# Kernel tuning notes

Hardware: AMD Instinct MI355X
Metric: run time of the kernel (lower is better)

Reference implementation:

```python
import jax, jax.numpy as jnp
import numpy as np

B, N, C, H = 16, 4096, 256, 4
D = C // H

def setup_inputs() -> dict:
    key = jax.random.key(0)
    ks = jax.random.split(key, 8)
    w = 0.01  # small init, mimics xavier_uniform gain=0.1
    x = jax.random.normal(ks[0], (B, N, C), jnp.float32)
    S = jax.random.normal(ks[1], (B, H, D, D), jnp.float32) * 0.1
    Wq = jax.random.normal(ks[2], (C, C), jnp.float32) * w
    Wk = jax.random.normal(ks[3], (C, C), jnp.float32) * w
    Wv = jax.random.normal(ks[4], (C, C), jnp.float32) * w
    Wb = jax.random.normal(ks[5], (H, C), jnp.float32) * w  # beta_proj (zeros in torch init; random for nontrivial math)
    Wo = jax.random.normal(ks[6], (C, C), jnp.float32) * w
    g_rms = jnp.ones((C,), jnp.float32)
    return {"x": x, "S": S, "Wq": Wq, "Wk": Wk, "Wv": Wv, "Wb": Wb, "Wo": Wo, "g_rms": g_rms}

def reference(x, S, Wq, Wk, Wv, Wb, Wo, g_rms):
    b, n, c = x.shape
    h = Wb.shape[0]
    d = c // h
    # projections -> (B,H,N,D)
    q = (x @ Wq.T).reshape(b, n, h, d).transpose(0, 2, 1, 3)
    k = (x @ Wk.T).reshape(b, n, h, d).transpose(0, 2, 1, 3)
    v = (x @ Wv.T).reshape(b, n, h, d).transpose(0, 2, 1, 3)
    # feature map + L2 normalize keys
    k = jax.nn.elu(k) + 1.0
    k = k / (jnp.linalg.norm(k, axis=-1, keepdims=True) + 1e-6)
    # per-head gates (B,H,N,1)
    beta = jax.nn.sigmoid(jnp.einsum('bnc,hc->bhn', x, Wb))[..., None]
    # decay + state read
    Sd = S * 0.95
    y = jnp.einsum('bhij,bhnj->bhni', Sd, q)
    pred = jnp.einsum('bhij,bhnj->bhni', Sd, k)
    # delta-rule write: outer(mean weighted error, mean key)
    w_err = jnp.mean(beta * (v - pred), axis=2)  # (B,H,D)
    w_key = jnp.mean(k, axis=2)                  # (B,H,D)
    S_new = jnp.clip(Sd + jnp.einsum('bhi,bhj->bhij', w_err, w_key), -10.0, 10.0)
    # merge heads, RMSNorm, output projection
    y = y.transpose(0, 2, 1, 3).reshape(b, n, c)
    y = y * jax.lax.rsqrt(jnp.mean(y * y, axis=-1, keepdims=True) + 1e-6) * g_rms
    out = y @ Wo.T
    return out, S_new
```

## Files before the change

kernel.cpp:

```cpp
#include <hip/hip_runtime.h>
#include <math.h>


typedef _Float16 f16;
typedef f16 f16x8 __attribute__((ext_vector_type(8)));
typedef f16 f16x4 __attribute__((ext_vector_type(4)));
typedef float f32x4 __attribute__((ext_vector_type(4)));

typedef const __attribute__((address_space(1))) void gvoid;
typedef __attribute__((address_space(3))) void svoid;

__device__ __forceinline__ void gload16(const void* g, void* l) {
  __builtin_amdgcn_global_load_lds((gvoid*)g, (svoid*)l, 16, 0, 0);
}

__device__ __forceinline__ f16x8 cvt8(const float* q) {
  float4 a = *(const float4*)q;
  float4 b = *(const float4*)(q + 4);
  f16x8 r;
  r[0] = (f16)a.x; r[1] = (f16)a.y; r[2] = (f16)a.z; r[3] = (f16)a.w;
  r[4] = (f16)b.x; r[5] = (f16)b.y; r[6] = (f16)b.z; r[7] = (f16)b.w;
  return r;
}

__global__ __launch_bounds__(256) void prep_w(
    const float* __restrict__ Wk, const float* __restrict__ Wo,
    const float* __restrict__ g, f16* __restrict__ Wkh,
    f16* __restrict__ Wogh) {
  int i = blockIdx.x * 256 + threadIdx.x;
#pragma unroll
  for (int j = 0; j < 4; ++j) {
    int idx = i + j * 16384;
    Wkh[idx] = (f16)Wk[idx];
    Wogh[idx] = (f16)(Wo[idx] * g[idx & 255]);
  }
}

__global__ __launch_bounds__(256) void beta_xbsum_h(
    const float* __restrict__ x, const float* __restrict__ Wb,
    float* __restrict__ betaArr, float* __restrict__ xbsum,
    f16* __restrict__ xh) {
  const int t = threadIdx.x;
  const int wave = t >> 6, lane = t & 63;
  const int b = blockIdx.x >> 6;
  const int tile = blockIdx.x & 63;
  float4 wb[4];
#pragma unroll
  for (int h = 0; h < 4; ++h) wb[h] = *(const float4*)(Wb + h * 256 + lane * 4);
  float xacc[4][4] = {};
  const size_t rowbase = (size_t)b * 4096 + tile * 64;
  __shared__ float bsh[4][64];
  float4 xv = *(const float4*)(x + (rowbase + wave) * 256 + lane * 4);
#pragma unroll 2
  for (int i = 0; i < 16; ++i) {
    int r = i * 4 + wave;
    float4 nx = xv;
    if (i < 15)
      nx = *(const float4*)(x + (rowbase + r + 4) * 256 + lane * 4);
    f16x4 hx;
    hx[0] = (f16)xv.x; hx[1] = (f16)xv.y; hx[2] = (f16)xv.z; hx[3] = (f16)xv.w;
    *(f16x4*)(xh + (rowbase + r) * 256 + lane * 4) = hx;
#pragma unroll
    for (int h = 0; h < 4; ++h) {
      float s = xv.x * wb[h].x + xv.y * wb[h].y + xv.z * wb[h].z + xv.w * wb[h].w;
#pragma unroll
      for (int off = 32; off; off >>= 1) s += __shfl_xor(s, off);
      float bh = 1.f / (1.f + __expf(-s));
      if (lane == h) bsh[h][r] = bh;
      xacc[h][0] += bh * xv.x; xacc[h][1] += bh * xv.y;
      xacc[h][2] += bh * xv.z; xacc[h][3] += bh * xv.w;
    }
    xv = nx;
  }
  __shared__ float xbp[4][4][256];
#pragma unroll
  for (int h = 0; h < 4; ++h)
#pragma unroll
    for (int j = 0; j < 4; ++j) xbp[wave][h][lane * 4 + j] = xacc[h][j];
  __syncthreads();
  {
    int h = t >> 6, r = t & 63;
    betaArr[((size_t)(b * 4 + h) << 12) + tile * 64 + r] = bsh[h][r];
  }
  for (int idx = t; idx < 1024; idx += 256) {
    int h = idx >> 8, c = idx & 255;
    float s = xbp[0][h][c] + xbp[1][h][c] + xbp[2][h][c] + xbp[3][h][c];
    atomicAdd(&xbsum[(b * 4 + h) * 256 + c], s);
  }
}

__global__ __launch_bounds__(256) void kgemm_h(
    const f16* __restrict__ xh, const f16* __restrict__ Wkh,
    const float* __restrict__ betaArr,
    float* __restrict__ ksum, float* __restrict__ kbsum) {
  __shared__ union {
    struct { f16 A[128][64]; f16 B[128][64]; } s;
    f16 K[128][128];
  } u;
  __shared__ float bstage[2][128];
  const int t = threadIdx.x;
  const int m0 = blockIdx.y * 128;
  const int n0 = blockIdx.x * 128;
  const int b = m0 >> 12;
  const int wave = t >> 6, lane = t & 63;
  const int wm = (wave >> 1) * 64, wn = (wave & 1) * 64;
  const int fr = lane & 15, fq = lane >> 4;
  const int fr7 = fr & 7;
  const int srow = lane >> 3;
  const int sc = (lane & 7) ^ srow;
  {
    int hh = t >> 7, r = t & 127;
    bstage[hh][r] =
        betaArr[((size_t)(b * 4 + (n0 >> 6) + hh) << 12) + (m0 & 4095) + r];
  }
  const char* Ab = (const char*)&u.s.A[0][0];
  const char* Bb = (const char*)&u.s.B[0][0];
  f32x4 acc[4][4] = {};
#pragma unroll 1
  for (int kt = 0; kt < 4; ++kt) {
    const int k0 = kt * 64;
#pragma unroll
    for (int j = 0; j < 4; ++j) {
      int c = j * 4 + wave;
      int row = c * 8 + srow;
      gload16(xh + (size_t)(m0 + row) * 256 + k0 + sc * 8, &u.s.A[0][0] + c * 512);
      gload16(Wkh + (size_t)(n0 + row) * 256 + k0 + sc * 8, &u.s.B[0][0] + c * 512);
    }
    __syncthreads();
#pragma unroll
    for (int ks = 0; ks < 2; ++ks) {
      const int p = ((ks * 4 + fq) ^ fr7) << 4;
      f16x8 afr[4], bfr[4];
#pragma unroll
      for (int mi = 0; mi < 4; ++mi)
        afr[mi] = *(const f16x8*)(Ab + (wm + mi * 16 + fr) * 128 + p);
#pragma unroll
      for (int ni = 0; ni < 4; ++ni)
        bfr[ni] = *(const f16x8*)(Bb + (wn + ni * 16 + fr) * 128 + p);
#pragma unroll
      for (int mi = 0; mi < 4; ++mi)
#pragma unroll
        for (int ni = 0; ni < 4; ++ni)
          acc[mi][ni] = __builtin_amdgcn_mfma_f32_16x16x32_f16(
              afr[mi], bfr[ni], acc[mi][ni], 0, 0, 0);
    }
    __syncthreads();
  }
#pragma unroll
  for (int mi = 0; mi < 4; ++mi)
#pragma unroll
    for (int rr = 0; rr < 4; ++rr) {
      float s = 0.f;
#pragma unroll
      for (int ni = 0; ni < 4; ++ni) {
        float v = acc[mi][ni][rr];
        v = v > 0.f ? v + 1.f : __expf(v);
        acc[mi][ni][rr] = v;
        s += v * v;
      }
#pragma unroll
      for (int off = 1; off < 16; off <<= 1) s += __shfl_xor(s, off);
      float inv = 1.f / (sqrtf(s) + 1e-6f);
#pragma unroll
      for (int ni = 0; ni < 4; ++ni) acc[mi][ni][rr] *= inv;
    }
#pragma unroll
  for (int mi = 0; mi < 4; ++mi)
#pragma unroll
    for (int ni = 0; ni < 4; ++ni)
#pragma unroll
      for (int rr = 0; rr < 4; ++rr)
        u.K[wm + mi * 16 + fq * 4 + rr][wn + ni * 16 + fr] = (f16)acc[mi][ni][rr];
  __syncthreads();
  if (t < 128) {
    const int c = t, hl = c >> 6;
    float sk = 0.f, skb = 0.f;
#pragma unroll 4
    for (int r = 0; r < 128; ++r) {
      float v = (float)u.K[r][c];
      float be = bstage[hl][r];
      sk += v;
      skb += be * v;
    }
    int gh = b * 4 + (n0 >> 6) + hl;
    atomicAdd(&ksum[gh * 64 + (c & 63)], sk);
    atomicAdd(&kbsum[gh * 64 + (c & 63)], skb);
  }
}

__global__ __launch_bounds__(256) void fold_M(
    const float* __restrict__ S, const float* __restrict__ Wq,
    f16* __restrict__ M) {
  const int bh = blockIdx.y;
  const int dq = blockIdx.x;
  const int h = bh & 3;
  const int t = threadIdx.x;
  const float* Sp = S + (size_t)bh * 4096 + dq * 8 * 64;
  const float* Wp = Wq + (size_t)h * 64 * 256 + t;
  float m[8] = {};
#pragma unroll 4
  for (int e = 0; e < 64; ++e) {
    float wv = Wp[e * 256];
#pragma unroll
    for (int dd = 0; dd < 8; ++dd) m[dd] += Sp[dd * 64 + e] * wv;
  }
  f16* Mb = M + (size_t)(bh >> 2) * 65536;
#pragma unroll
  for (int dd = 0; dd < 8; ++dd)
    Mb[(size_t)(h * 64 + dq * 8 + dd) * 256 + t] = (f16)(0.95f * m[dd]);
}

__global__ __launch_bounds__(256) void ygemm_h(
    const f16* __restrict__ xh, int m_base, const f16* __restrict__ M,
    f16* __restrict__ y, float* __restrict__ rowssq) {
  __shared__ f16 As[128][64];
  __shared__ f16 Bs[128][64];
  const int t = threadIdx.x;
  const int m0 = blockIdx.y * 128;
  const int n0 = blockIdx.x * 128;
  const int b = (m_base + m0) >> 12;
  const f16* Mb = M + (size_t)b * 65536;
  const int wave = t >> 6, lane = t & 63;
  const int wm = (wave >> 1) * 64, wn = (wave & 1) * 64;
  const int fr = lane & 15, fq = lane >> 4;
  const int fr7 = fr & 7;
  const int srow = lane >> 3;
  const int sc = (lane & 7) ^ srow;
  const char* Ab = (const char*)&As[0][0];
  const char* Bb = (const char*)&Bs[0][0];
  f32x4 acc[4][4] = {};
#pragma unroll 1
  for (int kt = 0; kt < 4; ++kt) {
    const int k0 = kt * 64;
#pragma unroll
    for (int j = 0; j < 4; ++j) {
      int c = j * 4 + wave;
      int row = c * 8 + srow;
      gload16(xh + (size_t)(m_base + m0 + row) * 256 + k0 + sc * 8,
              &As[0][0] + c * 512);
      gload16(Mb + (size_t)(n0 + row) * 256 + k0 + sc * 8, &Bs[0][0] + c * 512);
    }
    __syncthreads();
#pragma unroll
    for (int ks = 0; ks < 2; ++ks) {
      const int p = ((ks * 4 + fq) ^ fr7) << 4;
      f16x8 afr[4], bfr[4];
#pragma unroll
      for (int mi = 0; mi < 4; ++mi)
        afr[mi] = *(const f16x8*)(Ab + (wm + mi * 16 + fr) * 128 + p);
#pragma unroll
      for (int ni = 0; ni < 4; ++ni)
        bfr[ni] = *(const f16x8*)(Bb + (wn + ni * 16 + fr) * 128 + p);
#pragma unroll
      for (int mi = 0; mi < 4; ++mi)
#pragma unroll
        for (int ni = 0; ni < 4; ++ni)
          acc[mi][ni] = __builtin_amdgcn_mfma_f32_16x16x32_f16(
              afr[mi], bfr[ni], acc[mi][ni], 0, 0, 0);
    }
    __syncthreads();
  }
#pragma unroll
  for (int mi = 0; mi < 4; ++mi)
#pragma unroll
    for (int rr = 0; rr < 4; ++rr) {
      float s = 0.f;
#pragma unroll
      for (int ni = 0; ni < 4; ++ni) {
        float v = acc[mi][ni][rr];
        s += v * v;
        int row = m0 + wm + mi * 16 + fq * 4 + rr;
        int col = n0 + wn + ni * 16 + fr;
        y[(size_t)row * 256 + col] = (f16)v;
      }
#pragma unroll
      for (int off = 1; off < 16; off <<= 1) s += __shfl_xor(s, off);
      if (fr == 0)
        atomicAdd(&rowssq[m0 + wm + mi * 16 + fq * 4 + rr], s);
    }
}

__global__ __launch_bounds__(256) void ogemm_h(
    const f16* __restrict__ y, const float* __restrict__ rowssq,
    const f16* __restrict__ Wogh, float* __restrict__ out, int m_base) {
  __shared__ f16 As[128][64];
  __shared__ f16 Bs[128][64];
  __shared__ float rsl[128];
  const int t = threadIdx.x;
  const int m0 = blockIdx.y * 128;
  const int n0 = blockIdx.x * 128;
  const int wave = t >> 6, lane = t & 63;
  const int wm = (wave >> 1) * 64, wn = (wave & 1) * 64;
  const int fr = lane & 15, fq = lane >> 4;
  const int fr7 = fr & 7;
  const int srow = lane >> 3;
  const int sc = (lane & 7) ^ srow;
  const char* Ab = (const char*)&As[0][0];
  const char* Bb = (const char*)&Bs[0][0];
  if (t < 128) rsl[t] = rsqrtf(rowssq[m0 + t] * (1.f / 256.f) + 1e-6f);
  f32x4 acc[4][4] = {};
#pragma unroll 1
  for (int kt = 0; kt < 4; ++kt) {
    const int k0 = kt * 64;
#pragma unroll
    for (int j = 0; j < 4; ++j) {
      int c = j * 4 + wave;
      int row = c * 8 + srow;
      gload16(y + (size_t)(m0 + row) * 256 + k0 + sc * 8, &As[0][0] + c * 512);
      gload16(Wogh + (size_t)(n0 + row) * 256 + k0 + sc * 8, &Bs[0][0] + c * 512);
    }
    __syncthreads();
#pragma unroll
    for (int ks = 0; ks < 2; ++ks) {
      const int p = ((ks * 4 + fq) ^ fr7) << 4;
      f16x8 afr[4], bfr[4];
#pragma unroll
      for (int mi = 0; mi < 4; ++mi)
        afr[mi] = *(const f16x8*)(Ab + (wm + mi * 16 + fr) * 128 + p);
#pragma unroll
      for (int ni = 0; ni < 4; ++ni)
        bfr[ni] = *(const f16x8*)(Bb + (wn + ni * 16 + fr) * 128 + p);
#pragma unroll
      for (int mi = 0; mi < 4; ++mi)
#pragma unroll
        for (int ni = 0; ni < 4; ++ni)
          acc[mi][ni] = __builtin_amdgcn_mfma_f32_16x16x32_f16(
              afr[mi], bfr[ni], acc[mi][ni], 0, 0, 0);
    }
    __syncthreads();
  }
#pragma unroll
  for (int mi = 0; mi < 4; ++mi)
#pragma unroll
    for (int rr = 0; rr < 4; ++rr) {
      int lrow = wm + mi * 16 + fq * 4 + rr;
      float rs = rsl[lrow];
#pragma unroll
      for (int ni = 0; ni < 4; ++ni) {
        int row = m_base + m0 + lrow;
        int col = n0 + wn + ni * 16 + fr;
        out[(size_t)row * 256 + col] = rs * acc[mi][ni][rr];
      }
    }
}

__global__ __launch_bounds__(256) void beta_xbsum(
    const float* __restrict__ x, const float* __restrict__ Wb,
    float* __restrict__ betaArr, float* __restrict__ xbsum) {
  const int t = threadIdx.x;
  const int wave = t >> 6, lane = t & 63;
  const int b = blockIdx.x >> 6;
  const int tile = blockIdx.x & 63;
  float4 wb[4];
#pragma unroll
  for (int h = 0; h < 4; ++h) wb[h] = *(const float4*)(Wb + h * 256 + lane * 4);
  float xacc[4][4] = {};
  const size_t rowbase = (size_t)b * 4096 + tile * 64;
  __shared__ float bsh[4][64];
  float4 xv = *(const float4*)(x + (rowbase + wave) * 256 + lane * 4);
#pragma unroll 2
  for (int i = 0; i < 16; ++i) {
    int r = i * 4 + wave;
    float4 nx = xv;
    if (i < 15)
      nx = *(const float4*)(x + (rowbase + r + 4) * 256 + lane * 4);
#pragma unroll
    for (int h = 0; h < 4; ++h) {
      float s = xv.x * wb[h].x + xv.y * wb[h].y + xv.z * wb[h].z + xv.w * wb[h].w;
#pragma unroll
      for (int off = 32; off; off >>= 1) s += __shfl_xor(s, off);
      float bh = 1.f / (1.f + __expf(-s));
      if (lane == h) bsh[h][r] = bh;
      xacc[h][0] += bh * xv.x; xacc[h][1] += bh * xv.y;
      xacc[h][2] += bh * xv.z; xacc[h][3] += bh * xv.w;
    }
    xv = nx;
  }
  __shared__ float xbp[4][4][256];
#pragma unroll
  for (int h = 0; h < 4; ++h)
#pragma unroll
    for (int j = 0; j < 4; ++j) xbp[wave][h][lane * 4 + j] = xacc[h][j];
  __syncthreads();
  {
    int h = t >> 6, r = t & 63;
    betaArr[((size_t)(b * 4 + h) << 12) + tile * 64 + r] = bsh[h][r];
  }
  for (int idx = t; idx < 1024; idx += 256) {
    int h = idx >> 8, c = idx & 255;
    float s = xbp[0][h][c] + xbp[1][h][c] + xbp[2][h][c] + xbp[3][h][c];
    atomicAdd(&xbsum[(b * 4 + h) * 256 + c], s);
  }
}

__global__ __launch_bounds__(256) void kgemm_sums(
    const float* __restrict__ x, const float* __restrict__ Wk,
    const float* __restrict__ betaArr,
    float* __restrict__ ksum, float* __restrict__ kbsum) {
  __shared__ union {
    struct { f16 A[128][72]; f16 B[128][72]; } s;
    f16 K[128][132];
  } u;
  __shared__ float bstage[2][128];
  const int t = threadIdx.x;
  const int m0 = blockIdx.y * 128;
  const int n0 = blockIdx.x * 128;
  const int b = m0 >> 12;
  const int wave = t >> 6, lane = t & 63;
  const int wm = (wave >> 1) * 64, wn = (wave & 1) * 64;
  const int fr = lane & 15, fq = lane >> 4;
  {
    int hh = t >> 7, r = t & 127;
    bstage[hh][r] =
        betaArr[((size_t)(b * 4 + (n0 >> 6) + hh) << 12) + (m0 & 4095) + r];
  }
  f32x4 acc[4][4] = {};
#pragma unroll 1
  for (int kt = 0; kt < 4; ++kt) {
    const int k0 = kt * 64;
#pragma unroll
    for (int i = 0; i < 4; ++i) {
      int id = i * 256 + t;
      int row = id >> 3, cc = id & 7;
      *(f16x8*)&u.s.A[row][cc * 8] =
          cvt8(x + (size_t)(m0 + row) * 256 + k0 + cc * 8);
      *(f16x8*)&u.s.B[row][cc * 8] =
          cvt8(Wk + (size_t)(n0 + row) * 256 + k0 + cc * 8);
    }
    __syncthreads();
#pragma unroll
    for (int ks = 0; ks < 2; ++ks) {
      f16x8 afr[4], bfr[4];
#pragma unroll
      for (int mi = 0; mi < 4; ++mi)
        afr[mi] = *(const f16x8*)&u.s.A[wm + mi * 16 + fr][ks * 32 + fq * 8];
#pragma unroll
      for (int ni = 0; ni < 4; ++ni)
        bfr[ni] = *(const f16x8*)&u.s.B[wn + ni * 16 + fr][ks * 32 + fq * 8];
#pragma unroll
      for (int mi = 0; mi < 4; ++mi)
#pragma unroll
        for (int ni = 0; ni < 4; ++ni)
          acc[mi][ni] = __builtin_amdgcn_mfma_f32_16x16x32_f16(
              afr[mi], bfr[ni], acc[mi][ni], 0, 0, 0);
    }
    __syncthreads();
  }
#pragma unroll
  for (int mi = 0; mi < 4; ++mi)
#pragma unroll
    for (int rr = 0; rr < 4; ++rr) {
      float s = 0.f;
#pragma unroll
      for (int ni = 0; ni < 4; ++ni) {
        float v = acc[mi][ni][rr];
        v = v > 0.f ? v + 1.f : __expf(v);
        acc[mi][ni][rr] = v;
        s += v * v;
      }
#pragma unroll
      for (int off = 1; off < 16; off <<= 1) s += __shfl_xor(s, off);
      float inv = 1.f / (sqrtf(s) + 1e-6f);
#pragma unroll
      for (int ni = 0; ni < 4; ++ni) acc[mi][ni][rr] *= inv;
    }
#pragma unroll
  for (int mi = 0; mi < 4; ++mi)
#pragma unroll
    for (int ni = 0; ni < 4; ++ni)
#pragma unroll
      for (int rr = 0; rr < 4; ++rr)
        u.K[wm + mi * 16 + fq * 4 + rr][wn + ni * 16 + fr] = (f16)acc[mi][ni][rr];
  __syncthreads();
  if (t < 128) {
    const int c = t, hl = c >> 6;
    float sk = 0.f, skb = 0.f;
#pragma unroll 4
    for (int r = 0; r < 128; ++r) {
      float v = (float)u.K[r][c];
      float be = bstage[hl][r];
      sk += v;
      skb += be * v;
    }
    int gh = b * 4 + (n0 >> 6) + hl;
    atomicAdd(&ksum[gh * 64 + (c & 63)], sk);
    atomicAdd(&kbsum[gh * 64 + (c & 63)], skb);
  }
}

__global__ __launch_bounds__(256) void ygemm_ssq(
    const float* __restrict__ x, int m_base, const f16* __restrict__ M,
    f16* __restrict__ y, float* __restrict__ rowssq) {
  __shared__ f16 As[128][72];
  __shared__ f16 Bs[128][72];
  const int t = threadIdx.x;
  const int m0 = blockIdx.y * 128;
  const int n0 = blockIdx.x * 128;
  const int b = (m_base + m0) >> 12;
  const f16* Mb = M + (size_t)b * 65536;
  const int wave = t >> 6, lane = t & 63;
  const int wm = (wave >> 1) * 64, wn = (wave & 1) * 64;
  const int fr = lane & 15, fq = lane >> 4;
  f32x4 acc[4][4] = {};
#pragma unroll 1
  for (int kt = 0; kt < 4; ++kt) {
    const int k0 = kt * 64;
#pragma unroll
    for (int i = 0; i < 4; ++i) {
      int id = i * 256 + t;
      int row = id >> 3, cc = id & 7;
      *(f16x8*)&As[row][cc * 8] =
          cvt8(x + (size_t)(m_base + m0 + row) * 256 + k0 + cc * 8);
      *(uint4*)&Bs[row][cc * 8] =
          *(const uint4*)(Mb + (size_t)(n0 + row) * 256 + k0 + cc * 8);
    }
    __syncthreads();
#pragma unroll
    for (int ks = 0; ks < 2; ++ks) {
      f16x8 afr[4], bfr[4];
#pragma unroll
      for (int mi = 0; mi < 4; ++mi)
        afr[mi] = *(const f16x8*)&As[wm + mi * 16 + fr][ks * 32 + fq * 8];
#pragma unroll
      for (int ni = 0; ni < 4; ++ni)
        bfr[ni] = *(const f16x8*)&Bs[wn + ni * 16 + fr][ks * 32 + fq * 8];
#pragma unroll
      for (int mi = 0; mi < 4; ++mi)
#pragma unroll
        for (int ni = 0; ni < 4; ++ni)
          acc[mi][ni] = __builtin_amdgcn_mfma_f32_16x16x32_f16(
              afr[mi], bfr[ni], acc[mi][ni], 0, 0, 0);
    }
    __syncthreads();
  }
#pragma unroll
  for (int mi = 0; mi < 4; ++mi)
#pragma unroll
    for (int rr = 0; rr < 4; ++rr) {
      float s = 0.f;
#pragma unroll
      for (int ni = 0; ni < 4; ++ni) {
        float v = acc[mi][ni][rr];
        s += v * v;
        int row = m0 + wm + mi * 16 + fq * 4 + rr;
        int col = n0 + wn + ni * 16 + fr;
        y[(size_t)row * 256 + col] = (f16)v;
      }
#pragma unroll
      for (int off = 1; off < 16; off <<= 1) s += __shfl_xor(s, off);
      if (fr == 0)
        atomicAdd(&rowssq[m0 + wm + mi * 16 + fq * 4 + rr], s);
    }
}

__global__ __launch_bounds__(256) void ogemm_scaled(
    const f16* __restrict__ y, const float* __restrict__ rowssq,
    const float* __restrict__ g_rms, const float* __restrict__ Wo,
    float* __restrict__ out, int m_base) {
  __shared__ f16 As[128][72];
  __shared__ f16 Bs[128][72];
  const int t = threadIdx.x;
  const int m0 = blockIdx.y * 128;
  const int n0 = blockIdx.x * 128;
  const int wave = t >> 6, lane = t & 63;
  const int wm = (wave >> 1) * 64, wn = (wave & 1) * 64;
  const int fr = lane & 15, fq = lane >> 4;
  f32x4 acc[4][4] = {};
#pragma unroll 1
  for (int kt = 0; kt < 4; ++kt) {
    const int k0 = kt * 64;
#pragma unroll
    for (int i = 0; i < 4; ++i) {
      int id = i * 256 + t;
      int row = id >> 3, cc = id & 7;
      float rs = rsqrtf(rowssq[m0 + row] * (1.f / 256.f) + 1e-6f);
      const f16* yp = y + (size_t)(m0 + row) * 256 + k0 + cc * 8;
      const float* gp = g_rms + k0 + cc * 8;
      f16x8 a;
#pragma unroll
      for (int j = 0; j < 8; ++j) a[j] = (f16)((float)yp[j] * rs * gp[j]);
      *(f16x8*)&As[row][cc * 8] = a;
      *(f16x8*)&Bs[row][cc * 8] =
          cvt8(Wo + (size_t)(n0 + row) * 256 + k0 + cc * 8);
    }
    __syncthreads();
#pragma unroll
    for (int ks = 0; ks < 2; ++ks) {
      f16x8 afr[4], bfr[4];
#pragma unroll
      for (int mi = 0; mi < 4; ++mi)
        afr[mi] = *(const f16x8*)&As[wm + mi * 16 + fr][ks * 32 + fq * 8];
#pragma unroll
      for (int ni = 0; ni < 4; ++ni)
        bfr[ni] = *(const f16x8*)&Bs[wn + ni * 16 + fr][ks * 32 + fq * 8];
#pragma unroll
      for (int mi = 0; mi < 4; ++mi)
#pragma unroll
        for (int ni = 0; ni < 4; ++ni)
          acc[mi][ni] = __builtin_amdgcn_mfma_f32_16x16x32_f16(
              afr[mi], bfr[ni], acc[mi][ni], 0, 0, 0);
    }
    __syncthreads();
  }
#pragma unroll
  for (int mi = 0; mi < 4; ++mi)
#pragma unroll
    for (int ni = 0; ni < 4; ++ni)
#pragma unroll
      for (int rr = 0; rr < 4; ++rr) {
        int row = m_base + m0 + wm + mi * 16 + fq * 4 + rr;
        int col = n0 + wn + ni * 16 + fr;
        out[(size_t)row * 256 + col] = acc[mi][ni][rr];
      }
}

__global__ __launch_bounds__(256) void finalize_S(
    const float* __restrict__ S, const float* __restrict__ Wv,
    const float* __restrict__ xbsum, const float* __restrict__ ksum,
    const float* __restrict__ kbsum, float* __restrict__ Sout) {
  const int bh = blockIdx.x;
  const int h = bh & 3;
  const int t = threadIdx.x;
  const int wave = t >> 6, lane = t & 63;
  __shared__ float xb[256], kb[64], key[64], errv[64];
  xb[t] = xbsum[bh * 256 + t];
  if (t < 64) {
    kb[t] = kbsum[bh * 64 + t];
    key[t] = ksum[bh * 64 + t] * (1.f / 4096.f);
  }
  __syncthreads();
#pragma unroll 1
  for (int ri = 0; ri < 16; ++ri) {
    int i = wave * 16 + ri;
    float4 wv4 = *(const float4*)(Wv + (size_t)(h * 64 + i) * 256 + lane * 4);
    float4 xb4 = *(const float4*)(&xb[lane * 4]);
    float s = wv4.x * xb4.x + wv4.y * xb4.y + wv4.z * xb4.z + wv4.w * xb4.w;
    s -= 0.95f * S[(size_t)bh * 4096 + i * 64 + lane] * kb[lane];
#pragma unroll
    for (int off = 32; off; off >>= 1) s += __shfl_xor(s, off);
    if (lane == 0) errv[i] = s * (1.f / 4096.f);
  }
  __syncthreads();
  for (int idx = t; idx < 4096; idx += 256) {
    int i = idx >> 6, j = idx & 63;
    float v = 0.95f * S[(size_t)bh * 4096 + idx] + errv[i] * key[j];
    Sout[(size_t)bh * 4096 + idx] = fminf(10.f, fmaxf(-10.f, v));
  }
}

extern "C" void kernel_launch(void* const* d_in, const int* in_sizes, int n_in,
                              void* d_out, int out_size, void* d_ws, size_t ws_size,
                              hipStream_t stream) {
  const float* x  = (const float*)d_in[0];
  const float* S  = (const float*)d_in[1];
  const float* Wq = (const float*)d_in[2];
  const float* Wk = (const float*)d_in[3];
  const float* Wv = (const float*)d_in[4];
  const float* Wb = (const float*)d_in[5];
  const float* Wo = (const float*)d_in[6];
  const float* g  = (const float*)d_in[7];

  char* w = (char*)d_ws;
  float* betaArr = (float*)w;
  f16*   M       = (f16*)(w + 1048576);
  f16*   y       = (f16*)(w + 3145728);
  float* rowssq  = (float*)(w + 19922944);
  float* xbsum   = (float*)(w + 20185088);
  float* ksum    = (float*)(w + 20250624);
  float* kbsum   = (float*)(w + 20267008);
  f16*   xh      = (f16*)(w + 20283392);
  f16*   Wkh     = (f16*)(w + 53837824);
  f16*   Wogh    = (f16*)(w + 53968896);
  const size_t WS_NEED = 54099968ull;

  float* out  = (float*)d_out;
  float* Sout = out + (size_t)16 * 4096 * 256;

  hipMemsetAsync(w + 19922944, 0, 360448, stream);

  if (ws_size >= WS_NEED) {
    prep_w<<<64, 256, 0, stream>>>(Wk, Wo, g, Wkh, Wogh);
    beta_xbsum_h<<<1024, 256, 0, stream>>>(x, Wb, betaArr, xbsum, xh);
    kgemm_h<<<dim3(2, 512), 256, 0, stream>>>(xh, Wkh, betaArr, ksum, kbsum);
    fold_M<<<dim3(8, 64), 256, 0, stream>>>(S, Wq, M);
    for (int half = 0; half < 2; ++half) {
      int m_base = half * 32768;
      ygemm_h<<<dim3(2, 256), 256, 0, stream>>>(xh, m_base, M, y,
                                                rowssq + half * 32768);
      ogemm_h<<<dim3(2, 256), 256, 0, stream>>>(y, rowssq + half * 32768,
                                                Wogh, out, m_base);
    }
  } else {
    beta_xbsum<<<1024, 256, 0, stream>>>(x, Wb, betaArr, xbsum);
    kgemm_sums<<<dim3(2, 512), 256, 0, stream>>>(x, Wk, betaArr, ksum, kbsum);
    fold_M<<<dim3(8, 64), 256, 0, stream>>>(S, Wq, M);
    for (int half = 0; half < 2; ++half) {
      int m_base = half * 32768;
      ygemm_ssq<<<dim3(2, 256), 256, 0, stream>>>(x, m_base, M, y,
                                                  rowssq + half * 32768);
      ogemm_scaled<<<dim3(2, 256), 256, 0, stream>>>(y, rowssq + half * 32768,
                                                     g, Wo, out, m_base);
    }
  }
  finalize_S<<<64, 256, 0, stream>>>(S, Wv, xbsum, ksum, kbsum, Sout);
}
```

Before: 235.0 us.

## Fuse y-GEMM, RMSNorm and output GEMM into one kernel keeping y in LDS

Replaces the two-pass ygemm_h/ogemm_h pair (launched per half) with a single kernel where each block computes a full 64x256 row tile of y, reduces row sums of squares in shared memory, normalizes, stores y as f16 in swizzled LDS, and then runs the output GEMM against Wo from LDS. This removes the global round trip of y, the rowssq atomics and part of the memset, and cuts launch count. In exchange each block uses about 72KB of LDS and reloads all of M and Wo per 64-row tile, which lowers occupancy and raises L2 traffic. A leftover empty wave<2 block stays in the code.

```diff
diff --git a/kernel.cpp b/kernel.cpp
--- a/kernel.cpp
+++ b/kernel.cpp
@@ -210,35 +210,45 @@
     Mb[(size_t)(h * 64 + dq * 8 + dd) * 256 + t] = (f16)(0.95f * m[dd]);
 }
 
-__global__ __launch_bounds__(256) void ygemm_h(
-    const f16* __restrict__ xh, int m_base, const f16* __restrict__ M,
-    f16* __restrict__ y, float* __restrict__ rowssq) {
-  __shared__ f16 As[128][64];
-  __shared__ f16 Bs[128][64];
-  const int t = threadIdx.x;
-  const int m0 = blockIdx.y * 128;
-  const int n0 = blockIdx.x * 128;
-  const int b = (m_base + m0) >> 12;
+__global__ __launch_bounds__(256) void yogemm_h(
+    const f16* __restrict__ xh, const f16* __restrict__ M,
+    const f16* __restrict__ Wogh, float* __restrict__ out) {
+  __shared__ f16 Bst[256 * 64];
+  __shared__ f16 Ast[64 * 64];
+  __shared__ f16 yl[64 * 256];
+  __shared__ float ssq[4][64];
+  __shared__ float rs_l[64];
+  const int t = threadIdx.x;
+  const int m0 = blockIdx.x * 64;
+  const int b = m0 >> 12;
   const f16* Mb = M + (size_t)b * 65536;
   const int wave = t >> 6, lane = t & 63;
-  const int wm = (wave >> 1) * 64, wn = (wave & 1) * 64;
+  const int wn = wave * 64;
   const int fr = lane & 15, fq = lane >> 4;
   const int fr7 = fr & 7;
   const int srow = lane >> 3;
   const int sc = (lane & 7) ^ srow;
-  const char* Ab = (const char*)&As[0][0];
-  const char* Bb = (const char*)&Bs[0][0];
+  const char* Ab = (const char*)Ast;
+  const char* Bb = (const char*)Bst;
   f32x4 acc[4][4] = {};
 #pragma unroll 1
   for (int kt = 0; kt < 4; ++kt) {
     const int k0 = kt * 64;
-#pragma unroll
-    for (int j = 0; j < 4; ++j) {
+    if (wave < 2) {
+      int c = wave * 4 + (lane >> 4);
+      int l16 = lane & 15;
+    }
+#pragma unroll
+    for (int j = 0; j < 2; ++j) {
       int c = j * 4 + wave;
       int row = c * 8 + srow;
-      gload16(xh + (size_t)(m_base + m0 + row) * 256 + k0 + sc * 8,
-              &As[0][0] + c * 512);
-      gload16(Mb + (size_t)(n0 + row) * 256 + k0 + sc * 8, &Bs[0][0] + c * 512);
+      gload16(xh + (size_t)(m0 + row) * 256 + k0 + sc * 8, Ast + c * 512);
+    }
+#pragma unroll
+    for (int j = 0; j < 8; ++j) {
+      int c = j * 4 + wave;
+      int row = c * 8 + srow;
+      gload16(Mb + (size_t)row * 256 + k0 + sc * 8, Bst + c * 512);
     }
     __syncthreads();
 #pragma unroll
@@ -247,7 +257,7 @@
       f16x8 afr[4], bfr[4];
 #pragma unroll
       for (int mi = 0; mi < 4; ++mi)
-        afr[mi] = *(const f16x8*)(Ab + (wm + mi * 16 + fr) * 128 + p);
+        afr[mi] = *(const f16x8*)(Ab + (mi * 16 + fr) * 128 + p);
 #pragma unroll
       for (int ni = 0; ni < 4; ++ni)
         bfr[ni] = *(const f16x8*)(Bb + (wn + ni * 16 + fr) * 128 + p);
@@ -269,45 +279,44 @@
       for (int ni = 0; ni < 4; ++ni) {
         float v = acc[mi][ni][rr];
         s += v * v;
-        int row = m0 + wm + mi * 16 + fq * 4 + rr;
-        int col = n0 + wn + ni * 16 + fr;
-        y[(size_t)row * 256 + col] = (f16)v;
       }
 #pragma unroll
       for (int off = 1; off < 16; off <<= 1) s += __shfl_xor(s, off);
-      if (fr == 0)
-        atomicAdd(&rowssq[m0 + wm + mi * 16 + fq * 4 + rr], s);
-    }
-}
-
-__global__ __launch_bounds__(256) void ogemm_h(
-    const f16* __restrict__ y, const float* __restrict__ rowssq,
-    const f16* __restrict__ Wogh, float* __restrict__ out, int m_base) {
-  __shared__ f16 As[128][64];
-  __shared__ f16 Bs[128][64];
-  __shared__ float rsl[128];
-  const int t = threadIdx.x;
-  const int m0 = blockIdx.y * 128;
-  const int n0 = blockIdx.x * 128;
-  const int wave = t >> 6, lane = t & 63;
-  const int wm = (wave >> 1) * 64, wn = (wave & 1) * 64;
-  const int fr = lane & 15, fq = lane >> 4;
-  const int fr7 = fr & 7;
-  const int srow = lane >> 3;
-  const int sc = (lane & 7) ^ srow;
-  const char* Ab = (const char*)&As[0][0];
-  const char* Bb = (const char*)&Bs[0][0];
-  if (t < 128) rsl[t] = rsqrtf(rowssq[m0 + t] * (1.f / 256.f) + 1e-6f);
-  f32x4 acc[4][4] = {};
+      if (fr == 0) ssq[wave][mi * 16 + fq * 4 + rr] = s;
+    }
+  __syncthreads();
+  if (t < 64)
+    rs_l[t] = rsqrtf((ssq[0][t] + ssq[1][t] + ssq[2][t] + ssq[3][t]) *
+                         (1.f / 256.f) +
+                     1e-6f);
+  __syncthreads();
+#pragma unroll
+  for (int mi = 0; mi < 4; ++mi)
+#pragma unroll
+    for (int rr = 0; rr < 4; ++rr) {
+      int row = mi * 16 + fq * 4 + rr;
+      float rs = rs_l[row];
+      int r7 = row & 7;
+#pragma unroll
+      for (int ni = 0; ni < 4; ++ni) {
+        int col = wn + ni * 16 + fr;
+        int idx = row * 256 + ((((col >> 3) ^ r7) << 3) | (col & 7));
+        yl[idx] = (f16)(rs * acc[mi][ni][rr]);
+      }
+    }
+  __syncthreads();
+#pragma unroll
+  for (int mi = 0; mi < 4; ++mi)
+#pragma unroll
+    for (int ni = 0; ni < 4; ++ni) acc[mi][ni] = (f32x4){0.f, 0.f, 0.f, 0.f};
 #pragma unroll 1
   for (int kt = 0; kt < 4; ++kt) {
     const int k0 = kt * 64;
 #pragma unroll
-    for (int j = 0; j < 4; ++j) {
+    for (int j = 0; j < 8; ++j) {
       int c = j * 4 + wave;
       int row = c * 8 + srow;
-      gload16(y + (size_t)(m0 + row) * 256 + k0 + sc * 8, &As[0][0] + c * 512);
-      gload16(Wogh + (size_t)(n0 + row) * 256 + k0 + sc * 8, &Bs[0][0] + c * 512);
+      gload16(Wogh + (size_t)row * 256 + k0 + sc * 8, Bst + c * 512);
     }
     __syncthreads();
 #pragma unroll
@@ -315,8 +324,11 @@
       const int p = ((ks * 4 + fq) ^ fr7) << 4;
       f16x8 afr[4], bfr[4];
 #pragma unroll
-      for (int mi = 0; mi < 4; ++mi)
-        afr[mi] = *(const f16x8*)(Ab + (wm + mi * 16 + fr) * 128 + p);
+      for (int mi = 0; mi < 4; ++mi) {
+        int row = mi * 16 + fr;
+        int chunk = ((kt * 8 + ks * 4 + fq) ^ (row & 7)) << 4;
+        afr[mi] = *(const f16x8*)((const char*)yl + row * 512 + chunk);
+      }
 #pragma unroll
       for (int ni = 0; ni < 4; ++ni)
         bfr[ni] = *(const f16x8*)(Bb + (wn + ni * 16 + fr) * 128 + p);
@@ -332,16 +344,13 @@
 #pragma unroll
   for (int mi = 0; mi < 4; ++mi)
 #pragma unroll
-    for (int rr = 0; rr < 4; ++rr) {
-      int lrow = wm + mi * 16 + fq * 4 + rr;
-      float rs = rsl[lrow];
-#pragma unroll
-      for (int ni = 0; ni < 4; ++ni) {
-        int row = m_base + m0 + lrow;
-        int col = n0 + wn + ni * 16 + fr;
-        out[(size_t)row * 256 + col] = rs * acc[mi][ni][rr];
+    for (int ni = 0; ni < 4; ++ni)
+#pragma unroll
+      for (int rr = 0; rr < 4; ++rr) {
+        int row = m0 + mi * 16 + fq * 4 + rr;
+        int col = wn + ni * 16 + fr;
+        out[(size_t)row * 256 + col] = acc[mi][ni][rr];
       }
-    }
 }
 
 __global__ __launch_bounds__(256) void beta_xbsum(
@@ -676,21 +685,15 @@
   float* out  = (float*)d_out;
   float* Sout = out + (size_t)16 * 4096 * 256;
 
-  hipMemsetAsync(w + 19922944, 0, 360448, stream);
-
   if (ws_size >= WS_NEED) {
+    hipMemsetAsync(w + 20185088, 0, 98304, stream);
     prep_w<<<64, 256, 0, stream>>>(Wk, Wo, g, Wkh, Wogh);
     beta_xbsum_h<<<1024, 256, 0, stream>>>(x, Wb, betaArr, xbsum, xh);
     kgemm_h<<<dim3(2, 512), 256, 0, stream>>>(xh, Wkh, betaArr, ksum, kbsum);
     fold_M<<<dim3(8, 64), 256, 0, stream>>>(S, Wq, M);
-    for (int half = 0; half < 2; ++half) {
-      int m_base = half * 32768;
-      ygemm_h<<<dim3(2, 256), 256, 0, stream>>>(xh, m_base, M, y,
-                                                rowssq + half * 32768);
-      ogemm_h<<<dim3(2, 256), 256, 0, stream>>>(y, rowssq + half * 32768,
-                                                Wogh, out, m_base);
-    }
+    yogemm_h<<<1024, 256, 0, stream>>>(xh, M, Wogh, out);
   } else {
+    hipMemsetAsync(w + 19922944, 0, 360448, stream);
     beta_xbsum<<<1024, 256, 0, stream>>>(x, Wb, betaArr, xbsum);
     kgemm_sums<<<dim3(2, 512), 256, 0, stream>>>(x, Wk, betaArr, ksum, kbsum);
     fold_M<<<dim3(8, 64), 256, 0, stream>>>(S, Wq, M);
```

Result: faster. 225.7 us (-4.0%).
